# Optimization experiments

Measured on AMD Instinct MI355X. Metric: run time of the kernel, lower is better.

## Reference

```python
import jax, jax.numpy as jnp
import numpy as np

N, C, F_OUT, H, W, K = 16, 3, 64, 256, 256, 3


def setup_inputs() -> dict:
    key = jax.random.key(0)
    k1, k2, k3 = jax.random.split(key, 3)
    x = jax.random.normal(k1, (N, C, H, W), dtype=jnp.float32)
    # kaiming_uniform-ish init scale (faithful magnitudes, exact dist irrelevant)
    fan_in = C * K * K
    bound_w = jnp.sqrt(6.0 / fan_in)
    weight = jax.random.uniform(k2, (F_OUT, C, K, K), dtype=jnp.float32,
                                minval=-bound_w, maxval=bound_w)
    bound_b = 1.0 / jnp.sqrt(fan_in)
    bias = jax.random.uniform(k3, (F_OUT,), dtype=jnp.float32,
                              minval=-bound_b, maxval=bound_b)
    return {"input": x, "weight": weight, "bias": bias}


def _conv2dcq(x, weight, bias):
    # Faithful to the source: weight3 is overwritten per channel, so only the
    # LAST weight input-channel survives; FHEDot consumes input3[i][0], i.e.
    # only input channel 0's im2col patches. FHEDot is a plain dot product.
    n, c, h, w = x.shape
    f = weight.shape[0]
    w3 = weight[:, c - 1].reshape(f, K * K)          # (F, 9)
    x0 = x[:, 0]                                      # (N, H, W)
    ho, wo = h - K + 1, w - K + 1
    # im2col patches for the 3x3 valid window: (N, Ho, Wo, 9)
    patches = jnp.stack(
        [x0[:, a:a + ho, b:b + wo] for a in range(K) for b in range(K)],
        axis=-1)
    out = jnp.einsum('fk,nhwk->nfhw', w3, patches)    # (N, F, Ho, Wo)
    return out + bias[None, :, None, None]


def reference(input, weight, bias):
    return _conv2dcq(input, weight, bias)
```

## Files before the change

kernel.cpp:

```cpp
#include <hip/hip_runtime.h>

#define NN   16
#define CC   3
#define FOUT 64
#define HH   256
#define WW   256
#define KK   3
#define HO   254
#define WO   254

typedef float f32x4_a8 __attribute__((ext_vector_type(4), aligned(8)));

__global__ __launch_bounds__(256) void conv2dcq_kernel(
    const float* __restrict__ x,
    const float* __restrict__ weight,
    const float* __restrict__ bias,
    float* __restrict__ out)
{
    __shared__ __align__(16) float w_lds[FOUT][12];

    const int tid = threadIdx.x;
    for (int idx = tid; idx < FOUT * 10; idx += 256) {
        const int f = idx / 10, k = idx - f * 10;
        w_lds[f][k] = (k < 9)
            ? weight[f * (CC * KK * KK) + (CC - 1) * (KK * KK) + k]
            : bias[f];
    }
    __syncthreads();

    const int lane  = tid & 63;
    const int wave  = tid >> 6;
    const int gwave = blockIdx.x * 4 + wave;
    const int n  = gwave / HO;
    const int i  = gwave - n * HO;

    const int j = (lane < 63) ? 4 * lane : 250;

    const float* xp = x + (size_t)n * (CC * HH * WW) + (size_t)i * WW + j;
    float in[3][6];
    #pragma unroll
    for (int r = 0; r < 3; ++r) {
        const f32x4_a8 a = *(const f32x4_a8*)(xp + r * WW);
        const float2   c = *(const float2*)(xp + r * WW + 4);
        in[r][0] = a.x; in[r][1] = a.y; in[r][2] = a.z; in[r][3] = a.w;
        in[r][4] = c.x; in[r][5] = c.y;
    }

    float* op = out + (size_t)n * (FOUT * HO * WO) + (size_t)i * WO + j;

    #pragma unroll 4
    for (int f = 0; f < FOUT; ++f) {
        const f32x4_a8 w0 = *(const f32x4_a8*)(&w_lds[f][0]);
        const f32x4_a8 w1 = *(const f32x4_a8*)(&w_lds[f][4]);
        const float2   wb = *(const float2*)(&w_lds[f][8]);

        const float wv[9] = { w0.x, w0.y, w0.z, w0.w,
                              w1.x, w1.y, w1.z, w1.w, wb.x };
        float acc[4] = { wb.y, wb.y, wb.y, wb.y };
        #pragma unroll
        for (int a = 0; a < 3; ++a) {
            #pragma unroll
            for (int q = 0; q < 3; ++q) {
                const float wq = wv[a * 3 + q];
                #pragma unroll
                for (int c = 0; c < 4; ++c)
                    acc[c] = fmaf(wq, in[a][q + c], acc[c]);
            }
        }

        f32x4_a8 v; v.x = acc[0]; v.y = acc[1]; v.z = acc[2]; v.w = acc[3];
        *(f32x4_a8*)op = v;
        op += HO * WO;
    }
}

extern "C" void kernel_launch(void* const* d_in, const int* in_sizes, int n_in,
                              void* d_out, int out_size, void* d_ws, size_t ws_size,
                              hipStream_t stream) {
    const float* x      = (const float*)d_in[0];
    const float* weight = (const float*)d_in[1];
    const float* bias   = (const float*)d_in[2];
    float* out          = (float*)d_out;

    const int total_waves = NN * HO;
    const int blocks = total_waves / 4;
    conv2dcq_kernel<<<blocks, 256, 0, stream>>>(x, weight, bias, out);
}
```

Baseline: 285.7 us.

## Switch to grid-stride flat output chunks with 16-byte aligned stores

```diff
diff --git a/kernel.cpp b/kernel.cpp
--- a/kernel.cpp
+++ b/kernel.cpp
@@ -8,8 +8,12 @@
 #define KK   3
 #define HO   254
 #define WO   254
+#define PLANE  (HO * WO)
+#define NELEM  (NN * FOUT * PLANE)
+#define NCHUNK (NELEM / 4)
 
-typedef float f32x4_a8 __attribute__((ext_vector_type(4), aligned(8)));
+typedef float f32x4_a16 __attribute__((ext_vector_type(4), aligned(16)));
+typedef float f32x4_a8  __attribute__((ext_vector_type(4), aligned(8)));
 
 __global__ __launch_bounds__(256) void conv2dcq_kernel(
     const float* __restrict__ x,
@@ -18,7 +22,6 @@
     float* __restrict__ out)
 {
     __shared__ __align__(16) float w_lds[FOUT][12];
-
     const int tid = threadIdx.x;
     for (int idx = tid; idx < FOUT * 10; idx += 256) {
         const int f = idx / 10, k = idx - f * 10;
@@ -28,49 +31,60 @@
     }
     __syncthreads();
 
-    const int lane  = tid & 63;
-    const int wave  = tid >> 6;
-    const int gwave = blockIdx.x * 4 + wave;
-    const int n  = gwave / HO;
-    const int i  = gwave - n * HO;
+    const unsigned stride = gridDim.x * 256u;
+    for (unsigned c = blockIdx.x * 256u + (unsigned)tid; c < NCHUNK; c += stride) {
+        const unsigned e0    = c * 4u;
+        const unsigned plane = e0 / PLANE;
+        const unsigned rem   = e0 - plane * PLANE;
+        const unsigned i0    = rem / WO;
+        const unsigned j0    = rem - i0 * WO;
+        const unsigned n     = plane >> 6;
+        const unsigned f     = plane & 63u;
 
-    const int j = (lane < 63) ? 4 * lane : 250;
-
-    const float* xp = x + (size_t)n * (CC * HH * WW) + (size_t)i * WW + j;
-    float in[3][6];
-    #pragma unroll
-    for (int r = 0; r < 3; ++r) {
-        const f32x4_a8 a = *(const f32x4_a8*)(xp + r * WW);
-        const float2   c = *(const float2*)(xp + r * WW + 4);
-        in[r][0] = a.x; in[r][1] = a.y; in[r][2] = a.z; in[r][3] = a.w;
-        in[r][4] = c.x; in[r][5] = c.y;
-    }
-
-    float* op = out + (size_t)n * (FOUT * HO * WO) + (size_t)i * WO + j;
-
-    #pragma unroll 4
-    for (int f = 0; f < FOUT; ++f) {
-        const f32x4_a8 w0 = *(const f32x4_a8*)(&w_lds[f][0]);
-        const f32x4_a8 w1 = *(const f32x4_a8*)(&w_lds[f][4]);
-        const float2   wb = *(const float2*)(&w_lds[f][8]);
-
+        const f32x4_a16 w0 = *(const f32x4_a16*)&w_lds[f][0];
+        const f32x4_a16 w1 = *(const f32x4_a16*)&w_lds[f][4];
+        const float2    wb = *(const float2*)   &w_lds[f][8];
         const float wv[9] = { w0.x, w0.y, w0.z, w0.w,
                               w1.x, w1.y, w1.z, w1.w, wb.x };
-        float acc[4] = { wb.y, wb.y, wb.y, wb.y };
-        #pragma unroll
-        for (int a = 0; a < 3; ++a) {
+        const float bv = wb.y;
+
+        const float* xp = x + (size_t)n * (CC * HH * WW) + (size_t)i0 * WW + j0;
+        f32x4_a16 acc = { bv, bv, bv, bv };
+
+        if (j0 != 252u) {
             #pragma unroll
-            for (int q = 0; q < 3; ++q) {
-                const float wq = wv[a * 3 + q];
+            for (int r = 0; r < 3; ++r) {
+                const f32x4_a8 a = *(const f32x4_a8*)(xp + r * WW);
+                const float2   b = *(const float2*)  (xp + r * WW + 4);
+                const float win[6] = { a.x, a.y, a.z, a.w, b.x, b.y };
                 #pragma unroll
-                for (int c = 0; c < 4; ++c)
-                    acc[c] = fmaf(wq, in[a][q + c], acc[c]);
+                for (int dc = 0; dc < 3; ++dc) {
+                    const float wq = wv[r * 3 + dc];
+                    acc.x = fmaf(wq, win[dc + 0], acc.x);
+                    acc.y = fmaf(wq, win[dc + 1], acc.y);
+                    acc.z = fmaf(wq, win[dc + 2], acc.z);
+                    acc.w = fmaf(wq, win[dc + 3], acc.w);
+                }
+            }
+        } else {
+            #pragma unroll
+            for (int r = 0; r < 3; ++r) {
+                const f32x4_a16 u = *(const f32x4_a16*)(xp + r * WW);
+                const f32x4_a16 v = *(const f32x4_a16*)(xp + (r + 1) * WW - 252);
+                const float uu[4] = { u.x, u.y, u.z, u.w };
+                const float vv[4] = { v.x, v.y, v.z, v.w };
+                #pragma unroll
+                for (int dc = 0; dc < 3; ++dc) {
+                    const float wq = wv[r * 3 + dc];
+                    acc.x = fmaf(wq, uu[dc + 0], acc.x);
+                    acc.y = fmaf(wq, uu[dc + 1], acc.y);
+                    acc.z = fmaf(wq, vv[dc + 0], acc.z);
+                    acc.w = fmaf(wq, vv[dc + 1], acc.w);
+                }
             }
         }
 
-        f32x4_a8 v; v.x = acc[0]; v.y = acc[1]; v.z = acc[2]; v.w = acc[3];
-        *(f32x4_a8*)op = v;
-        op += HO * WO;
+        *(f32x4_a16*)(out + e0) = acc;
     }
 }
 
@@ -82,7 +96,5 @@
     const float* bias   = (const float*)d_in[2];
     float* out          = (float*)d_out;
 
-    const int total_waves = NN * HO;
-    const int blocks = total_waves / 4;
-    conv2dcq_kernel<<<blocks, 256, 0, stream>>>(x, weight, bias, out);
+    conv2dcq_kernel<<<2048, 256, 0, stream>>>(x, weight, bias, out);
 }
```

Measured after the change: 304.6 us. 1.07x slower.

## Compute two output rows per wave with 16-byte aligned loads/stores and swizzled wave mapping

Applied to the files above, without the earlier changes.

```diff
diff --git a/kernel.cpp b/kernel.cpp
--- a/kernel.cpp
+++ b/kernel.cpp
@@ -8,7 +8,9 @@
 #define KK   3
 #define HO   254
 #define WO   254
+#define PLANE (HO * WO)
 
+typedef float f32x4    __attribute__((ext_vector_type(4), aligned(16)));
 typedef float f32x4_a8 __attribute__((ext_vector_type(4), aligned(8)));
 
 __global__ __launch_bounds__(256) void conv2dcq_kernel(
@@ -28,49 +30,70 @@
     }
     __syncthreads();
 
-    const int lane  = tid & 63;
-    const int wave  = tid >> 6;
-    const int gwave = blockIdx.x * 4 + wave;
-    const int n  = gwave / HO;
-    const int i  = gwave - n * HO;
+    const int lane = tid & 63;
+    const int wave = tid >> 6;
 
-    const int j = (lane < 63) ? 4 * lane : 250;
+    const int g   = (int)blockIdx.x * 4 + wave;
+    const int swz = (g & 7) * 254 + (g >> 3);
+    const unsigned n  = (unsigned)swz / 127u;
+    const int      ip = swz - (int)n * 127;
+    const int      i0 = 2 * ip;
 
-    const float* xp = x + (size_t)n * (CC * HH * WW) + (size_t)i * WW + j;
-    float in[3][6];
+    const int colA = (lane < 63) ? 4 * lane     : 252;
+    const int colB = (lane < 63) ? 4 * lane + 4 : 0;
+
+    const float* xp = x + (size_t)n * (CC * HH * WW) + (size_t)i0 * WW;
+    f32x4 A[4], B[4];
+    #pragma unroll
+    for (int r = 0; r < 4; ++r) {
+        A[r] = *(const f32x4*)(xp + r * WW + colA);
+        B[r] = *(const f32x4*)(xp + r * WW + colB);
+    }
+
+    float winE[3][6], winO[3][6];
     #pragma unroll
     for (int r = 0; r < 3; ++r) {
-        const f32x4_a8 a = *(const f32x4_a8*)(xp + r * WW);
-        const float2   c = *(const float2*)(xp + r * WW + 4);
-        in[r][0] = a.x; in[r][1] = a.y; in[r][2] = a.z; in[r][3] = a.w;
-        in[r][4] = c.x; in[r][5] = c.y;
+        winE[r][0] = A[r][0]; winE[r][1] = A[r][1]; winE[r][2] = A[r][2];
+        winE[r][3] = A[r][3]; winE[r][4] = B[r][0]; winE[r][5] = B[r][1];
+        winO[r][0] = A[r+1][2]; winO[r][1] = A[r+1][3]; winO[r][2] = B[r+1][0];
+        winO[r][3] = B[r+1][1]; winO[r][4] = B[r+1][2]; winO[r][5] = B[r+1][3];
     }
 
-    float* op = out + (size_t)n * (FOUT * HO * WO) + (size_t)i * WO + j;
+    float* op = out + (size_t)n * (FOUT * PLANE) + (size_t)i0 * WO;
 
     #pragma unroll 4
     for (int f = 0; f < FOUT; ++f) {
-        const f32x4_a8 w0 = *(const f32x4_a8*)(&w_lds[f][0]);
-        const f32x4_a8 w1 = *(const f32x4_a8*)(&w_lds[f][4]);
-        const float2   wb = *(const float2*)(&w_lds[f][8]);
-
+        const f32x4  w0 = *(const f32x4*)(&w_lds[f][0]);
+        const f32x4  w1 = *(const f32x4*)(&w_lds[f][4]);
+        const float2 wb = *(const float2*)(&w_lds[f][8]);
         const float wv[9] = { w0.x, w0.y, w0.z, w0.w,
                               w1.x, w1.y, w1.z, w1.w, wb.x };
-        float acc[4] = { wb.y, wb.y, wb.y, wb.y };
+        const float bv = wb.y;
+
+        float accE[4] = { bv, bv, bv, bv };
+        float accO[4] = { bv, bv, bv, bv };
         #pragma unroll
-        for (int a = 0; a < 3; ++a) {
+        for (int dr = 0; dr < 3; ++dr)
             #pragma unroll
-            for (int q = 0; q < 3; ++q) {
-                const float wq = wv[a * 3 + q];
+            for (int dc = 0; dc < 3; ++dc) {
+                const float wq = wv[dr * 3 + dc];
                 #pragma unroll
-                for (int c = 0; c < 4; ++c)
-                    acc[c] = fmaf(wq, in[a][q + c], acc[c]);
+                for (int c = 0; c < 4; ++c) {
+                    accE[c] = fmaf(wq, winE[dr][dc + c], accE[c]);
+                    accO[c] = fmaf(wq, winO[dr][dc + c], accO[c]);
+                }
             }
+
+        if (lane < 63) {
+            f32x4 ve; ve.x=accE[0]; ve.y=accE[1]; ve.z=accE[2]; ve.w=accE[3];
+            f32x4 vo; vo.x=accO[0]; vo.y=accO[1]; vo.z=accO[2]; vo.w=accO[3];
+            *(f32x4*)(op + colA)          = ve;
+            *(f32x4*)(op + WO + colA + 2) = vo;
+        } else {
+            *(float2*)(op + 252) = make_float2(accE[0], accE[1]);
+            *(float2*)(op + WO)  = make_float2(accO[2], accO[3]);
         }
-
-        f32x4_a8 v; v.x = acc[0]; v.y = acc[1]; v.z = acc[2]; v.w = acc[3];
-        *(f32x4_a8*)op = v;
-        op += HO * WO;
+        op += PLANE;
     }
 }
 
@@ -82,7 +105,7 @@
     const float* bias   = (const float*)d_in[2];
     float* out          = (float*)d_out;
 
-    const int total_waves = NN * HO;
+    const int total_waves = NN * (HO / 2);
     const int blocks = total_waves / 4;
     conv2dcq_kernel<<<blocks, 256, 0, stream>>>(x, weight, bias, out);
 }
```

After: 280.6 us. Within noise of the previous version (-1.8%).
